# Optimization experiments

Hardware: AMD Instinct MI355X
Metric: run time of the kernel (lower is better)

Reference implementation:

```python
import jax, jax.numpy as jnp
import numpy as np

B, N, QD, D, S, H, K = 4, 1024, 320, 512, 1024, 8, 32
DH = D // H  # 64
EPS = 1e-5


def setup_inputs() -> dict:
    key = jax.random.key(0)
    ks = jax.random.split(key, 10)
    sc = 1.0 / np.sqrt(D)
    return {
        "query_states": jax.random.normal(ks[0], (B, N, QD), dtype=jnp.float32),
        "Wqp": jax.random.normal(ks[1], (D, QD), dtype=jnp.float32) / np.sqrt(QD),
        "mem_keys": jax.random.normal(ks[2], (S, D), dtype=jnp.float32),
        "mem_values": jax.random.normal(ks[3], (S, D), dtype=jnp.float32) * 0.1,
        "Wq": jax.random.normal(ks[4], (D, D), dtype=jnp.float32) * sc,
        "Wk": jax.random.normal(ks[5], (D, D), dtype=jnp.float32) * sc,
        "Wv": jax.random.normal(ks[6], (D, D), dtype=jnp.float32) * sc,
        "Wo": jax.random.normal(ks[7], (D, D), dtype=jnp.float32) * sc,
        "ln_g": jnp.ones((D,), dtype=jnp.float32),
        "ln_b": jnp.zeros((D,), dtype=jnp.float32),
        "Wout": jax.random.normal(ks[8], (QD, D), dtype=jnp.float32) * sc,
        "bout": jnp.zeros((QD,), dtype=jnp.float32),
    }


def _l2norm(x):
    return x / jnp.sqrt(jnp.sum(x * x, axis=-1, keepdims=True) + 1e-12)


def reference(query_states, Wqp, mem_keys, mem_values, Wq, Wk, Wv, Wo, ln_g, ln_b, Wout, bout):
    # project queries into memory space: [B,N,D]
    q = jnp.einsum("bnq,dq->bnd", query_states, Wqp)
    # normalize memory slots (normalize_slots=True)
    keys = _l2norm(mem_keys)    # [S,D]
    vals = _l2norm(mem_values)  # [S,D]
    # top-k memory-slot preselection over raw query-key scores
    scores = jnp.einsum("bnd,sd->bns", q, keys)          # [B,N,S]
    _, top_idx = jax.lax.top_k(scores, K)                  # [B,N,K]
    sel_k = jnp.take(keys, top_idx, axis=0)                # [B,N,K,D]
    sel_v = jnp.take(vals, top_idx, axis=0)                # [B,N,K,D]
    # multi-head cross-attention over gathered slots
    qh = jnp.einsum("bnd,ed->bne", q, Wq).reshape(B, N, H, DH)
    kh = jnp.einsum("bnkd,ed->bnke", sel_k, Wk).reshape(B, N, K, H, DH)
    vh = jnp.einsum("bnkd,ed->bnke", sel_v, Wv).reshape(B, N, K, H, DH)
    att = jnp.einsum("bnhd,bnkhd->bnhk", qh, kh) / jnp.sqrt(jnp.float32(DH))  # temperature=1.0
    w = jax.nn.softmax(att, axis=-1)                       # [B,N,H,K]
    ctx = jnp.einsum("bnhk,bnkhd->bnhd", w, vh).reshape(B, N, D)
    ctx = jnp.einsum("bnd,ed->bne", ctx, Wo)               # [B,N,D]
    # output projector: LayerNorm + Linear(memory_dim -> query_dim); dropout inactive (eval)
    mu = jnp.mean(ctx, axis=-1, keepdims=True)
    var = jnp.mean((ctx - mu) ** 2, axis=-1, keepdims=True)
    normed = (ctx - mu) / jnp.sqrt(var + EPS) * ln_g + ln_b
    out = jnp.einsum("bnd,qd->bnq", normed, Wout) + bout   # [B,N,QD]
    return out
```

## Files before the change

### kernel.cpp

```cpp
#include <hip/hip_runtime.h>


__device__ __forceinline__ float bf2f(unsigned short u) {
    return __uint_as_float(((unsigned int)u) << 16);
}
__device__ __forceinline__ unsigned short f2bf(float f) {
    unsigned int u = __float_as_uint(f);
    u += 0x7FFFu + ((u >> 16) & 1u);
    return (unsigned short)(u >> 16);
}
__device__ __forceinline__ int detect_bf(const void* g) {
    return ((*(const unsigned int*)g) & 0xFFFFu) != 0u;
}
__device__ __forceinline__ float ldg1(const void* p, size_t i, int bf) {
    return bf ? bf2f(((const unsigned short*)p)[i]) : ((const float*)p)[i];
}
__device__ __forceinline__ void ld4(const void* p, size_t i, int bf, float* o) {
    if (bf) {
        ushort4 v = *reinterpret_cast<const ushort4*>((const unsigned short*)p + i);
        o[0] = bf2f(v.x); o[1] = bf2f(v.y); o[2] = bf2f(v.z); o[3] = bf2f(v.w);
    } else {
        float4 v = *reinterpret_cast<const float4*>((const float*)p + i);
        o[0] = v.x; o[1] = v.y; o[2] = v.z; o[3] = v.w;
    }
}
__device__ __forceinline__ unsigned int fkey(float x) {
    unsigned int u = __float_as_uint(x);
    return (u & 0x80000000u) ? ~u : (u | 0x80000000u);
}
__device__ __forceinline__ float funkey(unsigned int k) {
    unsigned int u = (k & 0x80000000u) ? (k & 0x7FFFFFFFu) : ~k;
    return __uint_as_float(u);
}

typedef __attribute__((ext_vector_type(8))) short bf16x8;
typedef __attribute__((ext_vector_type(4))) float f32x4;
typedef __attribute__((ext_vector_type(4))) unsigned int u32x4;

__device__ __forceinline__ void split8(const float* x, u32x4& h, u32x4& l) {
#pragma unroll
    for (int j = 0; j < 4; j++) {
        float x0 = x[2 * j], x1 = x[2 * j + 1];
        unsigned int hp, lp;
        asm("v_cvt_pk_bf16_f32 %0, %1, %2" : "=v"(hp) : "v"(x0), "v"(x1));
        float h0 = __uint_as_float(hp << 16);
        float h1 = __uint_as_float(hp & 0xFFFF0000u);
        float l0 = x0 - h0, l1 = x1 - h1;
        asm("v_cvt_pk_bf16_f32 %0, %1, %2" : "=v"(lp) : "v"(l0), "v"(l1));
        h[j] = hp; l[j] = lp;
    }
}

__device__ __forceinline__ void gload16(const void* g, void* l) {
    __builtin_amdgcn_global_load_lds(
        (const __attribute__((address_space(1))) unsigned int*)g,
        (__attribute__((address_space(3))) unsigned int*)l,
        16, 0, 0);
}

__global__ __launch_bounds__(256) void prep_fused(
    const void* __restrict__ Wqp, const void* __restrict__ X,
    const void* __restrict__ gdet,
    float* __restrict__ WqpT,
    unsigned short* __restrict__ Xh, unsigned short* __restrict__ Xl)
{
    __shared__ float tile[32][36];
    const int bf = detect_bf(gdet);
    const int bid = blockIdx.x, t = threadIdx.x;
    if (bid < 160) {
        int tid = bid;
        int d0 = (tid & 15) * 32, q0 = (tid >> 4) * 32;
        int r = t >> 3, c = (t & 7) * 4;
        float v[4];
        ld4(Wqp, (size_t)(d0 + r) * 320 + q0 + c, bf, v);
#pragma unroll
        for (int i = 0; i < 4; i++) tile[r][c + i] = v[i];
        __syncthreads();
        float o[4];
#pragma unroll
        for (int i = 0; i < 4; i++) o[i] = tile[c + i][r];
        *reinterpret_cast<float4*>(&WqpT[(size_t)(q0 + r) * 512 + d0 + c]) =
            make_float4(o[0], o[1], o[2], o[3]);
    } else {
        int i = (bid - 160) * 256 + t;
        float v[8];
        ld4(X, (size_t)i * 8, bf, v);
        ld4(X, (size_t)i * 8 + 4, bf, v + 4);
        u32x4 h, l;
        split8(v, h, l);
        *reinterpret_cast<u32x4*>(Xh + (size_t)i * 8) = h;
        *reinterpret_cast<u32x4*>(Xl + (size_t)i * 8) = l;
    }
}

__global__ __launch_bounds__(256) void mfma_abt(
    const void* __restrict__ A, const void* __restrict__ B,
    const float* __restrict__ scale, float* __restrict__ C,
    const void* __restrict__ A2, const void* __restrict__ B2,
    const float* __restrict__ scale2, float* __restrict__ C2, int ysplit,
    const float2* __restrict__ stats, const void* __restrict__ g,
    const void* __restrict__ bvec, const void* __restrict__ bias,
    void* __restrict__ O,
    unsigned short* __restrict__ Hout, unsigned short* __restrict__ Lout,
    int hrow0a, int hrow0b,
    int N, int amode, int amode2, int abfon, int bbfon, int epi, int npass,
    const void* __restrict__ gdet)
{
    __shared__ __align__(16) short lds[12288];
    const int AHo = 0, ALo = 2048, BHo = 4096, BLo = 8192;
    const int flag = detect_bf(gdet);
    const int abf = abfon ? flag : 0;
    const int bbf = bbfon ? flag : 0;
    const int t = threadIdx.x;
    int by = blockIdx.y;
    const void* Ap = A; const void* Bp = B;
    const float* scp = scale; float* Cp = C;
    int hrow0 = hrow0a;
    int am = amode;
    if (ysplit && by >= ysplit) {
        Ap = A2; Bp = B2; scp = scale2; Cp = C2; by -= ysplit; hrow0 = hrow0b;
        am = amode2;
    }
    const int m0 = by * 32, n0 = blockIdx.x * 64;
    const int lane = t & 63, wv = t >> 6;
    const int wm = wv >> 1, wn = wv & 1;
    const int srow = t >> 3;
    const int sc8  = t & 7;

    int aoff[2], boff[2][2];
#pragma unroll
    for (int kk = 0; kk < 2; kk++) {
        int ra = wm * 16 + (lane & 15);
        int ca = kk * 4 + (lane >> 4);
        aoff[kk] = ra * 64 + ((ca ^ (ra & 7)) << 3);
    }
#pragma unroll
    for (int ni = 0; ni < 2; ni++)
#pragma unroll
        for (int kk = 0; kk < 2; kk++) {
            int rb = wn * 32 + ni * 16 + (lane & 15);
            int cb = kk * 4 + (lane >> 4);
            boff[ni][kk] = rb * 64 + ((cb ^ (rb & 7)) << 3);
        }

    const int addr0 = srow * 64 + ((sc8 ^ (srow & 7)) << 3);
    const int addr1 = addr0 + 32 * 64;

    float s0 = 1.0f;
    float2 st0 = make_float2(0.f, 1.f);
    if (am == 1) {
        s0 = scp ? scp[m0 + srow] : 1.0f;
    } else if (am == 3) {
        double ss = 0.0;
        for (int kb2 = 0; kb2 < 512; kb2 += 64) {
            float v8[8];
            ld4(Ap, (size_t)(m0 + srow) * 512 + kb2 + sc8 * 8,     abf, v8);
            ld4(Ap, (size_t)(m0 + srow) * 512 + kb2 + sc8 * 8 + 4, abf, v8 + 4);
#pragma unroll
            for (int j = 0; j < 8; j++) ss += (double)v8[j] * v8[j];
        }
        ss += __shfl_xor(ss, 1, 64);
        ss += __shfl_xor(ss, 2, 64);
        ss += __shfl_xor(ss, 4, 64);
        s0 = (float)(1.0 / sqrt(ss + 1e-12));
    } else if (am == 2) {
        if (stats) {
            st0 = stats[m0 + srow];
        } else {
            double s = 0.0, ss = 0.0;
            for (int kb2 = 0; kb2 < 512; kb2 += 64) {
                float v8[8];
                ld4(Ap, (size_t)(m0 + srow) * 512 + kb2 + sc8 * 8,     abf, v8);
                ld4(Ap, (size_t)(m0 + srow) * 512 + kb2 + sc8 * 8 + 4, abf, v8 + 4);
#pragma unroll
                for (int j = 0; j < 8; j++) {
                    s  += (double)v8[j];
                    ss += (double)v8[j] * v8[j];
                }
            }
            s  += __shfl_xor(s, 1, 64);  ss += __shfl_xor(ss, 1, 64);
            s  += __shfl_xor(s, 2, 64);  ss += __shfl_xor(ss, 2, 64);
            s  += __shfl_xor(s, 4, 64);  ss += __shfl_xor(ss, 4, 64);
            double mu = s / 512.0, var = ss / 512.0 - mu * mu;
            st0 = make_float2((float)mu, (float)(1.0 / sqrt(var + 1e-5)));
        }
    }

    f32x4 acc[2];
    acc[0] = (f32x4){0.f, 0.f, 0.f, 0.f};
    acc[1] = (f32x4){0.f, 0.f, 0.f, 0.f};

    float av0[8], bv0[8], bv1[8];
    {
        ld4(Ap, (size_t)(m0 + srow) * 512 + sc8 * 8,          abf, av0);
        ld4(Ap, (size_t)(m0 + srow) * 512 + sc8 * 8 + 4,      abf, av0 + 4);
        ld4(Bp, (size_t)(n0 + srow) * 512 + sc8 * 8,          bbf, bv0);
        ld4(Bp, (size_t)(n0 + srow) * 512 + sc8 * 8 + 4,      bbf, bv0 + 4);
        ld4(Bp, (size_t)(n0 + srow + 32) * 512 + sc8 * 8,     bbf, bv1);
        ld4(Bp, (size_t)(n0 + srow + 32) * 512 + sc8 * 8 + 4, bbf, bv1 + 4);
    }

    for (int ks = 0; ks < 8; ks++) {
        const int kb = ks * 64;
        float a0[8], b0[8], b1[8];
#pragma unroll
        for (int j = 0; j < 8; j++) { a0[j] = av0[j]; b0[j] = bv0[j]; b1[j] = bv1[j]; }
        if (am == 1 || am == 3) {
#pragma unroll
            for (int j = 0; j < 8; j++) a0[j] *= s0;
        } else if (am == 2) {
            float gv[8], bv8[8];
            ld4(g,    (size_t)(kb + sc8 * 8),     flag, gv);
            ld4(g,    (size_t)(kb + sc8 * 8 + 4), flag, gv + 4);
            ld4(bvec, (size_t)(kb + sc8 * 8),     flag, bv8);
            ld4(bvec, (size_t)(kb + sc8 * 8 + 4), flag, bv8 + 4);
#pragma unroll
            for (int j = 0; j < 8; j++)
                a0[j] = (a0[j] - st0.x) * st0.y * gv[j] + bv8[j];
        }
        u32x4 ah0, al0, bh0, bl0, bh1, bl1;
        split8(a0, ah0, al0);
        split8(b0, bh0, bl0); split8(b1, bh1, bl1);
        __syncthreads();
        *reinterpret_cast<u32x4*>(&lds[AHo + addr0]) = ah0;
        *reinterpret_cast<u32x4*>(&lds[ALo + addr0]) = al0;
        *reinterpret_cast<u32x4*>(&lds[BHo + addr0]) = bh0;
        *reinterpret_cast<u32x4*>(&lds[BHo + addr1]) = bh1;
        *reinterpret_cast<u32x4*>(&lds[BLo + addr0]) = bl0;
        *reinterpret_cast<u32x4*>(&lds[BLo + addr1]) = bl1;
        __syncthreads();
        if (ks < 7) {
            const int kn = kb + 64;
            ld4(Ap, (size_t)(m0 + srow) * 512 + kn + sc8 * 8,          abf, av0);
            ld4(Ap, (size_t)(m0 + srow) * 512 + kn + sc8 * 8 + 4,      abf, av0 + 4);
            ld4(Bp, (size_t)(n0 + srow) * 512 + kn + sc8 * 8,          bbf, bv0);
            ld4(Bp, (size_t)(n0 + srow) * 512 + kn + sc8 * 8 + 4,      bbf, bv0 + 4);
            ld4(Bp, (size_t)(n0 + srow + 32) * 512 + kn + sc8 * 8,     bbf, bv1);
            ld4(Bp, (size_t)(n0 + srow + 32) * 512 + kn + sc8 * 8 + 4, bbf, bv1 + 4);
        }
        for (int p = 0; p < npass; p++) {
            const int Ab = (p == 1 || p == 3) ? ALo : AHo;
            const int Bb = (p >= 2) ? BLo : BHo;
#pragma unroll
            for (int kk = 0; kk < 2; kk++) {
                bf16x8 af, bfr[2];
                af = *reinterpret_cast<const bf16x8*>(&lds[Ab + aoff[kk]]);
#pragma unroll
                for (int ni = 0; ni < 2; ni++)
                    bfr[ni] = *reinterpret_cast<const bf16x8*>(&lds[Bb + boff[ni][kk]]);
#pragma unroll
                for (int ni = 0; ni < 2; ni++)
                    acc[ni] = __builtin_amdgcn_mfma_f32_16x16x32_bf16(
                        af, bfr[ni], acc[ni], 0, 0, 0);
            }
        }
    }

    {
        int mbase = m0 + wm * 16 + (lane >> 4) * 4;
#pragma unroll
        for (int ni = 0; ni < 2; ni++) {
            int n = n0 + wn * 32 + ni * 16 + (lane & 15);
            if (epi == 0) {
#pragma unroll
                for (int r = 0; r < 4; r++) {
                    float v = acc[ni][r];
                    Cp[(size_t)(mbase + r) * N + n] = v;
                    if (Hout) {
                        unsigned short hb = f2bf(v);
                        unsigned short lb = f2bf(v - bf2f(hb));
                        size_t ho = (size_t)(hrow0 + mbase + r) * N + n;
                        Hout[ho] = hb;
                        Lout[ho] = lb;
                    }
                }
            } else {
                float bo = bias ? ldg1(bias, n, flag) : 0.f;
#pragma unroll
                for (int r = 0; r < 4; r++) {
                    float v = acc[ni][r] + bo;
                    size_t off = (size_t)(mbase + r) * N + n;
                    if (flag) ((unsigned short*)O)[off] = f2bf(v);
                    else      ((float*)O)[off] = v;
                }
            }
        }
    }
}

__global__ __launch_bounds__(256) void gemm_scqh(
    const unsigned short* __restrict__ Xh, const unsigned short* __restrict__ Xl,
    const unsigned short* __restrict__ Bh, const unsigned short* __restrict__ Bl,
    float* __restrict__ Sc, float* __restrict__ qh)
{
    __shared__ __align__(16) short lds[24576];
    const int AHo = 0, ALo = 8192, BHo = 16384, BLo = 20480;
    const int t = threadIdx.x;
    const int m0 = blockIdx.y * 128, n0 = blockIdx.x * 64;
    const int lane = t & 63, wv = t >> 6;
    const int wm = wv >> 1, wn = wv & 1;
    const int lr = lane >> 3;
    const int lc = lane & 7;

    int aoff[4][2], boff[2][2];
#pragma unroll
    for (int mi = 0; mi < 4; mi++)
#pragma unroll
        for (int kk = 0; kk < 2; kk++) {
            int ra = wm * 64 + mi * 16 + (lane & 15);
            int ca = kk * 4 + (lane >> 4);
            aoff[mi][kk] = ra * 64 + ((ca ^ (ra & 7)) << 3);
        }
#pragma unroll
    for (int ni = 0; ni < 2; ni++)
#pragma unroll
        for (int kk = 0; kk < 2; kk++) {
            int rb = wn * 32 + ni * 16 + (lane & 15);
            int cb = kk * 4 + (lane >> 4);
            boff[ni][kk] = rb * 64 + ((cb ^ (rb & 7)) << 3);
        }

    f32x4 acc[4][2];
#pragma unroll
    for (int mi = 0; mi < 4; mi++)
#pragma unroll
        for (int ni = 0; ni < 2; ni++)
            acc[mi][ni] = (f32x4){0.f, 0.f, 0.f, 0.f};

    char* smem = (char*)lds;

    for (int ks = 0; ks < 5; ks++) {
        const int kb = ks * 64;
        __syncthreads();
#pragma unroll
        for (int i = 0; i < 4; i++) {
            int r0 = wv * 32 + i * 8;
            int r  = r0 + lr;
            int sc = lc ^ (r & 7);
            size_t go = (size_t)(m0 + r) * 320 + kb + sc * 8;
            gload16(Xh + go, smem + (AHo << 1) + r0 * 128);
            gload16(Xl + go, smem + (ALo << 1) + r0 * 128);
        }
#pragma unroll
        for (int i = 0; i < 2; i++) {
            int r0 = wv * 16 + i * 8;
            int r  = r0 + lr;
            int sc = lc ^ (r & 7);
            size_t go = (size_t)(n0 + r) * 320 + kb + sc * 8;
            gload16(Bh + go, smem + (BHo << 1) + r0 * 128);
            gload16(Bl + go, smem + (BLo << 1) + r0 * 128);
        }
        __syncthreads();
#pragma unroll
        for (int p = 0; p < 3; p++) {
            const int Ab = (p == 1) ? ALo : AHo;
            const int Bb = (p == 2) ? BLo : BHo;
#pragma unroll
            for (int kk = 0; kk < 2; kk++) {
                bf16x8 af[4], bfr[2];
#pragma unroll
                for (int mi = 0; mi < 4; mi++)
                    af[mi] = *reinterpret_cast<const bf16x8*>(&lds[Ab + aoff[mi][kk]]);
#pragma unroll
                for (int ni = 0; ni < 2; ni++)
                    bfr[ni] = *reinterpret_cast<const bf16x8*>(&lds[Bb + boff[ni][kk]]);
#pragma unroll
                for (int mi = 0; mi < 4; mi++)
#pragma unroll
                    for (int ni = 0; ni < 2; ni++)
                        acc[mi][ni] = __builtin_amdgcn_mfma_f32_16x16x32_bf16(
                            af[mi], bfr[ni], acc[mi][ni], 0, 0, 0);
            }
        }
    }

#pragma unroll
    for (int mi = 0; mi < 4; mi++) {
        int mbase = m0 + wm * 64 + mi * 16 + (lane >> 4) * 4;
#pragma unroll
        for (int ni = 0; ni < 2; ni++) {
            int n = n0 + wn * 32 + ni * 16 + (lane & 15);
#pragma unroll
            for (int r = 0; r < 4; r++) {
                float v = acc[mi][ni][r];
                int m = mbase + r;
                if (n0 < 1024) Sc[(size_t)m * 1024 + n] = v;
                else           qh[(size_t)m * 512 + (n - 1024)] = v;
            }
        }
    }
}

__global__ __launch_bounds__(256) void topk_attn(
    const float* __restrict__ Sc, const void* __restrict__ X,
    const void* __restrict__ gdet, const float* __restrict__ KWf,
    const float* __restrict__ qh, const float* __restrict__ Kp,
    const float* __restrict__ Vp, float* __restrict__ ctx)
{
    __shared__ unsigned int srow[4][1024];
    __shared__ unsigned int scv[4][64];
    __shared__ int          sci[4][64];
    __shared__ int          sidx4[4][32];
    __shared__ float        sq[512];
    __shared__ float        sl[8][32];
    __shared__ float        sw[8][32];
    const int bf = detect_bf(gdet);
    const int t = threadIdx.x;
    const int w = t >> 6, lane = t & 63;
    const int row = blockIdx.x * 4 + w;
    const float* S = Sc + (size_t)row * 1024;

    unsigned int mn = 0xFFFFFFFFu, mx = 0u;
#pragma unroll
    for (int q = 0; q < 4; q++) {
        float4 v = *reinterpret_cast<const float4*>(&S[lane * 4 + q * 256]);
        uint4 k = make_uint4(fkey(v.x), fkey(v.y), fkey(v.z), fkey(v.w));
        *reinterpret_cast<uint4*>(&srow[w][lane * 4 + q * 256]) = k;
        mn = min(mn, min(min(k.x, k.y), min(k.z, k.w)));
        mx = max(mx, max(max(k.x, k.y), max(k.z, k.w)));
    }
    scv[w][lane] = 0u;
    sci[w][lane] = 0x7FFFFFFF;
#pragma unroll
    for (int o = 1; o < 64; o <<= 1) {
        mn = min(mn, __shfl_xor(mn, o, 64));
        mx = max(mx, __shfl_xor(mx, o, 64));
    }
    __syncthreads();

    unsigned int lo = mn;
    unsigned int hi = (mx == 0xFFFFFFFFu) ? 0xFFFFFFFFu : mx + 1u;
    int cnt_lo = 1024;
    while (cnt_lo > 48 && hi - lo > 1u) {
        unsigned int mid = lo + ((hi - lo) >> 1);
        int c = 0;
#pragma unroll
        for (int q = 0; q < 4; q++) {
            uint4 k = *reinterpret_cast<const uint4*>(&srow[w][lane * 4 + q * 256]);
            c += (k.x >= mid) + (k.y >= mid) + (k.z >= mid) + (k.w >= mid);
        }
#pragma unroll
        for (int o = 1; o < 64; o <<= 1) c += __shfl_xor(c, o, 64);
        if (c >= 33) { lo = mid; cnt_lo = c; }
        else hi = mid;
    }
    const unsigned int T = lo;

    int cl = 0;
#pragma unroll
    for (int q = 0; q < 4; q++) {
        uint4 k = *reinterpret_cast<const uint4*>(&srow[w][lane * 4 + q * 256]);
        cl += (k.x >= T) + (k.y >= T) + (k.z >= T) + (k.w >= T);
    }
    int inc = cl;
#pragma unroll
    for (int o = 1; o < 64; o <<= 1) {
        int y = __shfl_up(inc, o, 64);
        if (lane >= o) inc += y;
    }
    int pos = inc - cl;
#pragma unroll
    for (int q = 0; q < 4; q++) {
        uint4 k = *reinterpret_cast<const uint4*>(&srow[w][lane * 4 + q * 256]);
        int base = lane * 4 + q * 256;
        if (k.x >= T && pos < 64) { scv[w][pos] = k.x; sci[w][pos] = base + 0; pos++; }
        if (k.y >= T && pos < 64) { scv[w][pos] = k.y; sci[w][pos] = base + 1; pos++; }
        if (k.z >= T && pos < 64) { scv[w][pos] = k.z; sci[w][pos] = base + 2; pos++; }
        if (k.w >= T && pos < 64) { scv[w][pos] = k.w; sci[w][pos] = base + 3; pos++; }
    }
    __syncthreads();
    unsigned int cv = scv[w][lane];
    int          ci = sci[w][lane];
#pragma unroll
    for (int k = 2; k <= 64; k <<= 1) {
#pragma unroll
        for (int jj = k >> 1; jj > 0; jj >>= 1) {
            unsigned int ov = __shfl_xor(cv, jj, 64);
            int          oi = __shfl_xor(ci, jj, 64);
            bool up = ((lane & k) == 0);
            bool takemax = (((lane & jj) == 0) == up);
            bool othergreater = (ov > cv) || (ov == cv && oi < ci);
            if (takemax == othergreater) { cv = ov; ci = oi; }
        }
    }
    float v31 = funkey(__shfl(cv, 31, 64));
    float v32 = funkey(__shfl(cv, 32, 64));
    int sel = ci;
    if (!(v31 - v32 > 2.5e-4f)) {
        size_t xb = (size_t)row * 320;
        bool active = (lane < 48) && (ci != 0x7FFFFFFF);
        int cidx = active ? ci : 0x7FFFFFFF;
        const float* kr = KWf + (size_t)(active ? ci : 0) * 320;
        double s = 0.0;
#pragma unroll 4
        for (int d = 0; d < 320; d++) {
            float xd = ldg1(X, xb + d, bf);
            s += (double)xd * (double)kr[d];
        }
        if (!active) s = -1.0e300;
#pragma unroll
        for (int k = 2; k <= 64; k <<= 1) {
#pragma unroll
            for (int jj = k >> 1; jj > 0; jj >>= 1) {
                double os = __shfl_xor(s, jj, 64);
                int    oi = __shfl_xor(cidx, jj, 64);
                bool up = ((lane & k) == 0);
                bool takemax = (((lane & jj) == 0) == up);
                bool og = (os > s) || (os == s && oi < cidx);
                if (takemax == og) { s = os; cidx = oi; }
            }
        }
        sel = cidx;
    }
    if (lane < 32) {
        int v = sel;
        sidx4[w][lane] = (v < 0) ? 0 : (v > 1023 ? 1023 : v);
    }
    __syncthreads();

    for (int r4 = 0; r4 < 4; r4++) {
        const int arow = blockIdx.x * 4 + r4;
        if (t < 128)
            *reinterpret_cast<float4*>(&sq[t * 4]) =
                *reinterpret_cast<const float4*>(&qh[(size_t)arow * 512 + t * 4]);
        __syncthreads();

        float4 q0 = *reinterpret_cast<const float4*>(&sq[lane * 8]);
        float4 q1 = *reinterpret_cast<const float4*>(&sq[lane * 8 + 4]);
        int h = lane >> 3;
#pragma unroll
        for (int i = 0; i < 8; i++) {
            int s = w * 8 + i;
            const float* kp = Kp + (size_t)sidx4[r4][s] * 512 + lane * 8;
            float4 k0 = *reinterpret_cast<const float4*>(kp);
            float4 k1 = *reinterpret_cast<const float4*>(kp + 4);
            float p = q0.x * k0.x + q0.y * k0.y + q0.z * k0.z + q0.w * k0.w
                    + q1.x * k1.x + q1.y * k1.y + q1.z * k1.z + q1.w * k1.w;
            p += __shfl_xor(p, 1, 64);
            p += __shfl_xor(p, 2, 64);
            p += __shfl_xor(p, 4, 64);
            if ((lane & 7) == 0) sl[h][s] = p * 0.125f;
        }
        __syncthreads();

        int hh = t >> 5, kk = t & 31;
        float logit = sl[hh][kk];
        float m = -1e30f;
#pragma unroll
        for (int i = 0; i < 32; i++) m = fmaxf(m, sl[hh][i]);
        float ssum = 0.f;
#pragma unroll
        for (int i = 0; i < 32; i++) ssum += __expf(sl[hh][i] - m);
        sw[hh][kk] = __expf(logit - m) / ssum;
        __syncthreads();

        int c = t * 2, hc = c >> 6;
        float ax = 0.f, ay = 0.f;
#pragma unroll
        for (int k2 = 0; k2 < 32; k2++) {
            float2 vv = *reinterpret_cast<const float2*>(
                &Vp[(size_t)sidx4[r4][k2] * 512 + c]);
            float wgt = sw[hc][k2];
            ax += wgt * vv.x; ay += wgt * vv.y;
        }
        *reinterpret_cast<float2*>(&ctx[(size_t)arow * 512 + c]) =
            make_float2(ax, ay);
        __syncthreads();
    }
}

extern "C" void kernel_launch(void* const* d_in, const int* in_sizes, int n_in,
                              void* d_out, int out_size, void* d_ws, size_t ws_size,
                              hipStream_t stream)
{
    const void* X    = d_in[0];
    const void* Wqp  = d_in[1];
    const void* keys = d_in[2];
    const void* vals = d_in[3];
    const void* Wq   = d_in[4];
    const void* Wk   = d_in[5];
    const void* Wv   = d_in[6];
    const void* Wo   = d_in[7];
    const void* ln_g = d_in[8];
    const void* ln_b = d_in[9];
    const void* Wout = d_in[10];
    const void* bout = d_in[11];

    float* ws = (float*)d_ws;
    float*  Sc     = ws;
    float*  co     = ws;
    float*  Yreg   = ws + 2097152;
    float*  qh     = ws + 4194304;
    float*  Mf     = ws + 6291456;
    float*  Kp     = ws + 6291456;
    float*  KWf    = ws + 6815744;
    float*  WqpT   = ws + 7340032;
    unsigned short* Xh  = (unsigned short*)(ws + 8388608);
    unsigned short* Xl  = (unsigned short*)(ws + 9043968);
    unsigned short* Bh  = (unsigned short*)(ws + 9699328);
    unsigned short* Bl  = (unsigned short*)(ws + 9945088);
    float*  Vp     = ws + 10190848;
    float*  ctx    = Yreg;

    prep_fused<<<800, 256, 0, stream>>>(Wqp, X, ln_g, WqpT, Xh, Xl);
    mfma_abt<<<dim3(5, 48), 256, 0, stream>>>(
        keys, WqpT, nullptr, KWf, Wq, WqpT, nullptr, Mf, 32,
        nullptr, nullptr, nullptr, nullptr, nullptr,
        Bh, Bl, 0, 1024,
        320, 3, 0, 1, 0, 0, 4, ln_g);
    gemm_scqh<<<dim3(24, 32), 256, 0, stream>>>(Xh, Xl, Bh, Bl, Sc, qh);
    mfma_abt<<<dim3(8, 64), 256, 0, stream>>>(
        keys, Wk, nullptr, Kp, vals, Wv, nullptr, Vp, 32,
        nullptr, nullptr, nullptr, nullptr, nullptr,
        nullptr, nullptr, 0, 0,
        512, 3, 3, 1, 1, 0, 3, ln_g);
    topk_attn<<<1024, 256, 0, stream>>>(Sc, X, ln_g, KWf, qh, Kp, Vp, ctx);
    mfma_abt<<<dim3(8, 128), 256, 0, stream>>>(
        ctx, Wo, nullptr, co, nullptr, nullptr, nullptr, nullptr, 0,
        nullptr, nullptr, nullptr, nullptr, nullptr,
        nullptr, nullptr, 0, 0,
        512, 0, 0, 0, 1, 0, 3, ln_g);
    mfma_abt<<<dim3(5, 128), 256, 0, stream>>>(
        co, Wout, nullptr, nullptr, nullptr, nullptr, nullptr, nullptr, 0,
        nullptr, ln_g, ln_b, bout, d_out,
        nullptr, nullptr, 0, 0,
        320, 2, 0, 0, 1, 1, 3, ln_g);
}
```

Before: 243.8 us.

## Split fused top-k/attention kernel into separate select and per-row attention kernels

Splits the fused top-k selection plus attention kernel into two kernels. topk_select writes the 32 chosen indices per row to a workspace buffer and exits early when no tie-break refinement is needed. attn_kernel then runs one block per row (4096 blocks) instead of looping over four rows with block-wide barriers. The aim is to stop the slow fp64 tie-break path from stalling the whole block's attention work, and to raise parallelism in the attention phase. The cost is an extra launch and a round trip of the index buffer through global memory.

```diff
diff --git a/kernel.cpp b/kernel.cpp
--- a/kernel.cpp
+++ b/kernel.cpp
@@ -391,22 +391,16 @@
     }
 }
 
-__global__ __launch_bounds__(256) void topk_attn(
+__global__ __launch_bounds__(256) void topk_select(
     const float* __restrict__ Sc, const void* __restrict__ X,
     const void* __restrict__ gdet, const float* __restrict__ KWf,
-    const float* __restrict__ qh, const float* __restrict__ Kp,
-    const float* __restrict__ Vp, float* __restrict__ ctx)
+    int* __restrict__ idx)
 {
     __shared__ unsigned int srow[4][1024];
     __shared__ unsigned int scv[4][64];
     __shared__ int          sci[4][64];
-    __shared__ int          sidx4[4][32];
-    __shared__ float        sq[512];
-    __shared__ float        sl[8][32];
-    __shared__ float        sw[8][32];
     const int bf = detect_bf(gdet);
-    const int t = threadIdx.x;
-    const int w = t >> 6, lane = t & 63;
+    const int w = threadIdx.x >> 6, lane = threadIdx.x & 63;
     const int row = blockIdx.x * 4 + w;
     const float* S = Sc + (size_t)row * 1024;
 
@@ -485,88 +479,94 @@
     }
     float v31 = funkey(__shfl(cv, 31, 64));
     float v32 = funkey(__shfl(cv, 32, 64));
-    int sel = ci;
-    if (!(v31 - v32 > 2.5e-4f)) {
-        size_t xb = (size_t)row * 320;
-        bool active = (lane < 48) && (ci != 0x7FFFFFFF);
-        int cidx = active ? ci : 0x7FFFFFFF;
-        const float* kr = KWf + (size_t)(active ? ci : 0) * 320;
-        double s = 0.0;
+    if (v31 - v32 > 2.5e-4f) {
+        if (lane < 32) idx[(size_t)row * 32 + lane] = ci;
+        return;
+    }
+    size_t xb = (size_t)row * 320;
+    bool active = (lane < 48) && (ci != 0x7FFFFFFF);
+    int cidx = active ? ci : 0x7FFFFFFF;
+    const float* kr = KWf + (size_t)(active ? ci : 0) * 320;
+    double s = 0.0;
 #pragma unroll 4
-        for (int d = 0; d < 320; d++) {
-            float xd = ldg1(X, xb + d, bf);
-            s += (double)xd * (double)kr[d];
-        }
-        if (!active) s = -1.0e300;
-#pragma unroll
-        for (int k = 2; k <= 64; k <<= 1) {
-#pragma unroll
-            for (int jj = k >> 1; jj > 0; jj >>= 1) {
-                double os = __shfl_xor(s, jj, 64);
-                int    oi = __shfl_xor(cidx, jj, 64);
-                bool up = ((lane & k) == 0);
-                bool takemax = (((lane & jj) == 0) == up);
-                bool og = (os > s) || (os == s && oi < cidx);
-                if (takemax == og) { s = os; cidx = oi; }
-            }
-        }
-        sel = cidx;
-    }
-    if (lane < 32) {
-        int v = sel;
-        sidx4[w][lane] = (v < 0) ? 0 : (v > 1023 ? 1023 : v);
+    for (int d = 0; d < 320; d++) {
+        float xd = ldg1(X, xb + d, bf);
+        s += (double)xd * (double)kr[d];
+    }
+    if (!active) s = -1.0e300;
+#pragma unroll
+    for (int k = 2; k <= 64; k <<= 1) {
+#pragma unroll
+        for (int jj = k >> 1; jj > 0; jj >>= 1) {
+            double os = __shfl_xor(s, jj, 64);
+            int    oi = __shfl_xor(cidx, jj, 64);
+            bool up = ((lane & k) == 0);
+            bool takemax = (((lane & jj) == 0) == up);
+            bool og = (os > s) || (os == s && oi < cidx);
+            if (takemax == og) { s = os; cidx = oi; }
+        }
+    }
+    if (lane < 32) idx[(size_t)row * 32 + lane] = cidx;
+}
+
+__global__ __launch_bounds__(256) void attn_kernel(
+    const float* __restrict__ qh, const float* __restrict__ Kp,
+    const float* __restrict__ Vp, const int* __restrict__ idx,
+    float* __restrict__ ctx)
+{
+    __shared__ float sq[512];
+    __shared__ int   sidx[32];
+    __shared__ float sl[8][32];
+    __shared__ float sw[8][32];
+    int row = blockIdx.x, t = threadIdx.x;
+    int w = t >> 6, l = t & 63;
+    if (t < 128)
+        *reinterpret_cast<float4*>(&sq[t * 4]) =
+            *reinterpret_cast<const float4*>(&qh[(size_t)row * 512 + t * 4]);
+    if (t < 32) {
+        int v = idx[(size_t)row * 32 + t];
+        sidx[t] = (v < 0) ? 0 : (v > 1023 ? 1023 : v);
     }
     __syncthreads();
 
-    for (int r4 = 0; r4 < 4; r4++) {
-        const int arow = blockIdx.x * 4 + r4;
-        if (t < 128)
-            *reinterpret_cast<float4*>(&sq[t * 4]) =
-                *reinterpret_cast<const float4*>(&qh[(size_t)arow * 512 + t * 4]);
-        __syncthreads();
-
-        float4 q0 = *reinterpret_cast<const float4*>(&sq[lane * 8]);
-        float4 q1 = *reinterpret_cast<const float4*>(&sq[lane * 8 + 4]);
-        int h = lane >> 3;
-#pragma unroll
-        for (int i = 0; i < 8; i++) {
-            int s = w * 8 + i;
-            const float* kp = Kp + (size_t)sidx4[r4][s] * 512 + lane * 8;
-            float4 k0 = *reinterpret_cast<const float4*>(kp);
-            float4 k1 = *reinterpret_cast<const float4*>(kp + 4);
-            float p = q0.x * k0.x + q0.y * k0.y + q0.z * k0.z + q0.w * k0.w
-                    + q1.x * k1.x + q1.y * k1.y + q1.z * k1.z + q1.w * k1.w;
-            p += __shfl_xor(p, 1, 64);
-            p += __shfl_xor(p, 2, 64);
-            p += __shfl_xor(p, 4, 64);
-            if ((lane & 7) == 0) sl[h][s] = p * 0.125f;
-        }
-        __syncthreads();
-
-        int hh = t >> 5, kk = t & 31;
-        float logit = sl[hh][kk];
-        float m = -1e30f;
-#pragma unroll
-        for (int i = 0; i < 32; i++) m = fmaxf(m, sl[hh][i]);
-        float ssum = 0.f;
-#pragma unroll
-        for (int i = 0; i < 32; i++) ssum += __expf(sl[hh][i] - m);
-        sw[hh][kk] = __expf(logit - m) / ssum;
-        __syncthreads();
-
-        int c = t * 2, hc = c >> 6;
-        float ax = 0.f, ay = 0.f;
-#pragma unroll
-        for (int k2 = 0; k2 < 32; k2++) {
-            float2 vv = *reinterpret_cast<const float2*>(
-                &Vp[(size_t)sidx4[r4][k2] * 512 + c]);
-            float wgt = sw[hc][k2];
-            ax += wgt * vv.x; ay += wgt * vv.y;
-        }
-        *reinterpret_cast<float2*>(&ctx[(size_t)arow * 512 + c]) =
-            make_float2(ax, ay);
-        __syncthreads();
-    }
+    float4 q0 = *reinterpret_cast<const float4*>(&sq[l * 8]);
+    float4 q1 = *reinterpret_cast<const float4*>(&sq[l * 8 + 4]);
+    int h = l >> 3;
+#pragma unroll
+    for (int i = 0; i < 8; i++) {
+        int s = w * 8 + i;
+        const float* kp = Kp + (size_t)sidx[s] * 512 + l * 8;
+        float4 k0 = *reinterpret_cast<const float4*>(kp);
+        float4 k1 = *reinterpret_cast<const float4*>(kp + 4);
+        float p = q0.x * k0.x + q0.y * k0.y + q0.z * k0.z + q0.w * k0.w
+                + q1.x * k1.x + q1.y * k1.y + q1.z * k1.z + q1.w * k1.w;
+        p += __shfl_xor(p, 1, 64);
+        p += __shfl_xor(p, 2, 64);
+        p += __shfl_xor(p, 4, 64);
+        if ((l & 7) == 0) sl[h][s] = p * 0.125f;
+    }
+    __syncthreads();
+
+    int hh = t >> 5, kk = t & 31;
+    float logit = sl[hh][kk];
+    float m = -1e30f;
+#pragma unroll
+    for (int i = 0; i < 32; i++) m = fmaxf(m, sl[hh][i]);
+    float ssum = 0.f;
+#pragma unroll
+    for (int i = 0; i < 32; i++) ssum += __expf(sl[hh][i] - m);
+    sw[hh][kk] = __expf(logit - m) / ssum;
+    __syncthreads();
+
+    int c = t * 2, hc = c >> 6;
+    float ax = 0.f, ay = 0.f;
+#pragma unroll
+    for (int k2 = 0; k2 < 32; k2++) {
+        float2 vv = *reinterpret_cast<const float2*>(&Vp[(size_t)sidx[k2] * 512 + c]);
+        float wgt = sw[hc][k2];
+        ax += wgt * vv.x; ay += wgt * vv.y;
+    }
+    *reinterpret_cast<float2*>(&ctx[(size_t)row * 512 + c]) = make_float2(ax, ay);
 }
 
 extern "C" void kernel_launch(void* const* d_in, const int* in_sizes, int n_in,
@@ -595,6 +595,7 @@
     float*  Kp     = ws + 6291456;
     float*  KWf    = ws + 6815744;
     float*  WqpT   = ws + 7340032;
+    int*    idx    = (int*)(ws + 7995392);
     unsigned short* Xh  = (unsigned short*)(ws + 8388608);
     unsigned short* Xl  = (unsigned short*)(ws + 9043968);
     unsigned short* Bh  = (unsigned short*)(ws + 9699328);
@@ -609,12 +610,13 @@
         Bh, Bl, 0, 1024,
         320, 3, 0, 1, 0, 0, 4, ln_g);
     gemm_scqh<<<dim3(24, 32), 256, 0, stream>>>(Xh, Xl, Bh, Bl, Sc, qh);
+    topk_select<<<1024, 256, 0, stream>>>(Sc, X, ln_g, KWf, idx);
     mfma_abt<<<dim3(8, 64), 256, 0, stream>>>(
         keys, Wk, nullptr, Kp, vals, Wv, nullptr, Vp, 32,
         nullptr, nullptr, nullptr, nullptr, nullptr,
         nullptr, nullptr, 0, 0,
         512, 3, 3, 1, 1, 0, 3, ln_g);
-    topk_attn<<<1024, 256, 0, stream>>>(Sc, X, ln_g, KWf, qh, Kp, Vp, ctx);
+    attn_kernel<<<4096, 256, 0, stream>>>(qh, Kp, Vp, idx, ctx);
     mfma_abt<<<dim3(8, 128), 256, 0, stream>>>(
         ctx, Wo, nullptr, co, nullptr, nullptr, nullptr, nullptr, 0,
         nullptr, nullptr, nullptr, nullptr, nullptr,
```

Result: faster. 237.4 us (-2.6%).
